# Kernel optimization log

Measured on AMD Instinct MI355X. Metric: run time of the kernel, lower is better.

## Reference

```python
import jax, jax.numpy as jnp
import numpy as np

N, K, A = 4096, 64, 8      # nodes, level-2 paths per node, attrs per l2-neighbor
D = 128                    # embed_dim
NU, NR, NA = 100000, 32, 5000  # user vocab, rating vocab, attribute vocab


def setup_inputs() -> dict:
    key = jax.random.key(0)
    ks = jax.random.split(key, 12)
    s = 0.02
    return dict(
        nodes=jax.random.randint(ks[0], (N,), 0, NU),
        paths_rel=jax.random.randint(ks[1], (N, K, 2), 0, NR),
        paths_nbr=jax.random.randint(ks[2], (N, K), 0, NU),
        attrs=jax.random.randint(ks[3], (N, K, A), 0, NA),
        u2e=jax.random.normal(ks[4], (NU, D), dtype=jnp.float32) * s,
        r2e=jax.random.normal(ks[5], (NR, D), dtype=jnp.float32) * s,
        ua2e=jax.random.normal(ks[6], (NA, D), dtype=jnp.float32) * s,
        W1=jax.random.normal(ks[7], (4 * D, 2 * D), dtype=jnp.float32) * s,
        b1=jnp.zeros((2 * D,), jnp.float32),
        W2=jax.random.normal(ks[8], (2 * D, D), dtype=jnp.float32) * s,
        b2=jnp.zeros((D,), jnp.float32),
        A1=jax.random.normal(ks[9], (2 * D, D), dtype=jnp.float32) * s,
        ab1=jnp.zeros((D,), jnp.float32),
        A2=jax.random.normal(ks[10], (D, D), dtype=jnp.float32) * s,
        ab2=jnp.zeros((D,), jnp.float32),
        A3=jax.random.normal(ks[11], (D, 1), dtype=jnp.float32) * s,
        ab3=jnp.zeros((1,), jnp.float32),
    )


def reference(nodes, paths_rel, paths_nbr, attrs, u2e, r2e, ua2e,
              W1, b1, W2, b2, A1, ab1, A2, ab2, A3, ab3):
    # per-path embedding gathers
    r1 = r2e[paths_rel[..., 0]]           # [N,K,D]
    r2 = r2e[paths_rel[..., 1]]           # [N,K,D]
    ne = u2e[paths_nbr]                   # [N,K,D]
    ae = ua2e[attrs].sum(axis=2)          # [N,K,A,D] -> [N,K,D] (uvAttrEmbedding sum)
    # concat + 2-layer MLP (w_r1, w_r2)
    x = jnp.concatenate([r1, r2, ne, ae], axis=-1)   # [N,K,4D]
    h = jax.nn.relu(x @ W1 + b1)                     # [N,K,2D]
    h = jax.nn.relu(h @ W2 + b2)                     # [N,K,D]
    # attention vs self embedding
    self_e = u2e[nodes]                              # [N,D]
    c = jnp.concatenate(
        [h, jnp.broadcast_to(self_e[:, None, :], h.shape)], axis=-1)  # [N,K,2D]
    a = jax.nn.relu(c @ A1 + ab1)
    a = jax.nn.relu(a @ A2 + ab2)
    logits = (a @ A3 + ab3)[..., 0]                  # [N,K]
    w = jax.nn.softmax(logits, axis=1)
    # attention-weighted reduce over paths
    return jnp.einsum('nk,nkd->nd', w, h)            # [N,D]
```

## Files before the change

### kernel.cpp

```cpp
#include <hip/hip_runtime.h>
#include <hip/hip_bf16.h>

#define NN 4096
#define KK 64
#define AA 8
#define DD 128

#define R1_SIZE   17408
#define XH_STRIDE 264
#define A_STRIDE  136
#define A2_OFF    8704
#define H2_STRIDE 136

typedef __bf16 bf16x8 __attribute__((ext_vector_type(8)));
typedef short  s16x8  __attribute__((ext_vector_type(8)));
typedef float  f32x4  __attribute__((ext_vector_type(4)));

__device__ __forceinline__ short f2bf(float f) {
    unsigned u = __builtin_bit_cast(unsigned, f);
    u += 0x7FFFu + ((u >> 16) & 1u);
    return (short)(u >> 16);
}
__device__ __forceinline__ float bf2f(short s) {
    unsigned u = ((unsigned)(unsigned short)s) << 16;
    return __builtin_bit_cast(float, u);
}
__device__ __forceinline__ void store_bf8(short* dst, float4 a, float4 b) {
    s16x8 v;
    v[0] = f2bf(a.x); v[1] = f2bf(a.y); v[2] = f2bf(a.z); v[3] = f2bf(a.w);
    v[4] = f2bf(b.x); v[5] = f2bf(b.y); v[6] = f2bf(b.z); v[7] = f2bf(b.w);
    *(s16x8*)dst = v;
}

__global__ void pack_all(const float* __restrict__ W1, const float* __restrict__ W2,
                         const float* __restrict__ A1, const float* __restrict__ A2,
                         short* __restrict__ W1p, short* __restrict__ W2p,
                         short* __restrict__ A1p, short* __restrict__ A2p)
{
    int t = blockIdx.x * 256 + threadIdx.x;
    const float* src; short* dst; int Ncols, ksl, idx;
    if (t < 131072)      { src = W1; dst = W1p; Ncols = 256; ksl = 4; idx = t; }
    else if (t < 163840) { src = W2; dst = W2p; Ncols = 128; ksl = 3; idx = t - 131072; }
    else if (t < 180224) { src = A1; dst = A1p; Ncols = 128; ksl = 2; idx = t - 163840; }
    else                 { src = A2; dst = A2p; Ncols = 128; ksl = 2; idx = t - 180224; }
    int j     = idx & 7;
    int lane  = (idx >> 3) & 63;
    int fi    = idx >> 9;
    int kstep = fi & ((1 << ksl) - 1);
    int ntile = fi >> ksl;
    int k  = kstep * 32 + (lane >> 4) * 8 + j;
    int nn = ntile * 16 + (lane & 15);
    dst[idx] = f2bf(src[(size_t)k * Ncols + nn]);
}

__global__ void prep_s1(const int* __restrict__ nodes, const float* __restrict__ u2e,
                        const float* __restrict__ A1, const float* __restrict__ ab1,
                        float* __restrict__ s1g)
{
    __shared__ float row[DD];
    const int n = blockIdx.x, c = threadIdx.x;
    const int node = nodes[n];
    row[c] = u2e[(size_t)node * DD + c];
    __syncthreads();
    float acc = ab1[c];
#pragma unroll 8
    for (int i = 0; i < DD; ++i)
        acc = fmaf(row[i], A1[(size_t)(DD + i) * DD + c], acc);
    s1g[(size_t)n * DD + c] = acc;
}

__launch_bounds__(256, 3)
__global__ void l2agg_mfma(
    const int* __restrict__ paths_rel,
    const int* __restrict__ paths_nbr,
    const int* __restrict__ attrs,
    const float* __restrict__ u2e,
    const float* __restrict__ r2e,
    const float* __restrict__ ua2e,
    const float* __restrict__ b1,
    const float* __restrict__ b2,
    const float* __restrict__ ab2,
    const float* __restrict__ A3,
    const float* __restrict__ ab3,
    const short* __restrict__ W1p,
    const short* __restrict__ W2p,
    const short* __restrict__ A1p,
    const short* __restrict__ A2p,
    const float* __restrict__ s1g,
    float* __restrict__ out)
{
    __shared__ short reg1[R1_SIZE];
    __shared__ short h2s[KK * H2_STRIDE];
    __shared__ int   idx_lds[KK * AA + KK];
    float* logits = (float*)&reg1[0];
    float* wts    = (float*)&reg1[128];

    const int n    = blockIdx.x;
    const int tid  = threadIdx.x;
    const int lane = tid & 63;
    const int wv   = tid >> 6;
    const int mr   = lane & 15;
    const int q    = lane >> 4;

    {
        const int* ab = attrs + (size_t)n * KK * AA;
        __builtin_amdgcn_global_load_lds(
            (const __attribute__((address_space(1))) void*)(ab + wv * 128 + lane),
            (__attribute__((address_space(3))) void*)(idx_lds + wv * 128), 4, 0, 0);
        __builtin_amdgcn_global_load_lds(
            (const __attribute__((address_space(1))) void*)(ab + wv * 128 + 64 + lane),
            (__attribute__((address_space(3))) void*)(idx_lds + wv * 128 + 64), 4, 0, 0);
        if (wv == 0) {
            const int* nb = paths_nbr + (size_t)n * KK;
            __builtin_amdgcn_global_load_lds(
                (const __attribute__((address_space(1))) void*)(nb + lane),
                (__attribute__((address_space(3))) void*)(idx_lds + 512), 4, 0, 0);
        }
    }

#pragma unroll
    for (int pass = 0; pass < 4; ++pass) {
        const int p  = pass * 16 + (tid >> 4);
        const int t  = tid & 15;
        const int o  = t * 8;
        const int pk = n * KK + p;
        const int i0 = paths_rel[pk * 2 + 0];
        const int i1 = paths_rel[pk * 2 + 1];
        float4 r1a = *(const float4*)&r2e[(size_t)i0 * DD + o];
        float4 r1b = *(const float4*)&r2e[(size_t)i0 * DD + o + 4];
        float4 r2a = *(const float4*)&r2e[(size_t)i1 * DD + o];
        float4 r2b = *(const float4*)&r2e[(size_t)i1 * DD + o + 4];
        store_bf8(&reg1[p * XH_STRIDE + o], r1a, r1b);
        store_bf8(&reg1[p * XH_STRIDE + 128 + o], r2a, r2b);
    }
    __syncthreads();

    const short* W1b = W1p + wv * 32768 + lane * 8;
    f32x4 acc1[4][4] = {};
    bf16x8 bfc[4], bfn[4];
#pragma unroll
    for (int nt = 0; nt < 4; ++nt) bfc[nt] = *(const bf16x8*)&W1b[nt * 8192];
#pragma unroll
    for (int ks = 0; ks < 8; ++ks) {
#pragma unroll
        for (int nt = 0; nt < 4; ++nt)
            bfn[nt] = *(const bf16x8*)&W1b[nt * 8192 + (ks + 1) * 512];
        bf16x8 af[4];
#pragma unroll
        for (int mt = 0; mt < 4; ++mt)
            af[mt] = *(const bf16x8*)&reg1[(mt * 16 + mr) * XH_STRIDE + ks * 32 + q * 8];
#pragma unroll
        for (int nt = 0; nt < 4; ++nt)
#pragma unroll
            for (int mt = 0; mt < 4; ++mt)
                acc1[mt][nt] = __builtin_amdgcn_mfma_f32_16x16x32_bf16(af[mt], bfc[nt], acc1[mt][nt], 0, 0, 0);
#pragma unroll
        for (int nt = 0; nt < 4; ++nt) bfc[nt] = bfn[nt];
    }
    __syncthreads();

#pragma unroll
    for (int pass = 0; pass < 4; ++pass) {
        const int p  = pass * 16 + (tid >> 4);
        const int t  = tid & 15;
        const int o  = t * 8;
        const int nb = idx_lds[512 + p];
        float4 nea = *(const float4*)&u2e[(size_t)nb * DD + o];
        float4 neb = *(const float4*)&u2e[(size_t)nb * DD + o + 4];
        float4 aea = make_float4(0.f, 0.f, 0.f, 0.f);
        float4 aeb = make_float4(0.f, 0.f, 0.f, 0.f);
#pragma unroll
        for (int a = 0; a < AA; ++a) {
            const int ai = idx_lds[p * AA + a];
            float4 va = *(const float4*)&ua2e[(size_t)ai * DD + o];
            float4 vb = *(const float4*)&ua2e[(size_t)ai * DD + o + 4];
            aea.x += va.x; aea.y += va.y; aea.z += va.z; aea.w += va.w;
            aeb.x += vb.x; aeb.y += vb.y; aeb.z += vb.z; aeb.w += vb.w;
        }
        store_bf8(&reg1[p * XH_STRIDE + o], nea, neb);
        store_bf8(&reg1[p * XH_STRIDE + 128 + o], aea, aeb);
    }
    __syncthreads();

#pragma unroll
    for (int ks = 8; ks < 16; ++ks) {
        if (ks < 15) {
#pragma unroll
            for (int nt = 0; nt < 4; ++nt)
                bfn[nt] = *(const bf16x8*)&W1b[nt * 8192 + (ks + 1) * 512];
        }
        bf16x8 af[4];
#pragma unroll
        for (int mt = 0; mt < 4; ++mt)
            af[mt] = *(const bf16x8*)&reg1[(mt * 16 + mr) * XH_STRIDE + (ks - 8) * 32 + q * 8];
#pragma unroll
        for (int nt = 0; nt < 4; ++nt)
#pragma unroll
            for (int mt = 0; mt < 4; ++mt)
                acc1[mt][nt] = __builtin_amdgcn_mfma_f32_16x16x32_bf16(af[mt], bfc[nt], acc1[mt][nt], 0, 0, 0);
        if (ks < 15) {
#pragma unroll
            for (int nt = 0; nt < 4; ++nt) bfc[nt] = bfn[nt];
        }
    }

    const short* W2b = W2p + wv * 8192 + lane * 8;
    bf16x8 g2c[2], g2n[2];
    g2c[0] = *(const bf16x8*)&W2b[0];
    g2c[1] = *(const bf16x8*)&W2b[4096];
    __syncthreads();

#pragma unroll
    for (int nt = 0; nt < 4; ++nt) {
        const int col = (wv * 4 + nt) * 16 + mr;
        const float bb = b1[col];
#pragma unroll
        for (int mt = 0; mt < 4; ++mt)
#pragma unroll
            for (int r = 0; r < 4; ++r)
                reg1[(mt * 16 + q * 4 + r) * XH_STRIDE + col] =
                    f2bf(fmaxf(acc1[mt][nt][r] + bb, 0.f));
    }
    __syncthreads();

    f32x4 acc2[4][2] = {};
#pragma unroll
    for (int ks = 0; ks < 8; ++ks) {
        if (ks < 7) {
            g2n[0] = *(const bf16x8*)&W2b[(ks + 1) * 512];
            g2n[1] = *(const bf16x8*)&W2b[4096 + (ks + 1) * 512];
        }
        bf16x8 af[4];
#pragma unroll
        for (int mt = 0; mt < 4; ++mt)
            af[mt] = *(const bf16x8*)&reg1[(mt * 16 + mr) * XH_STRIDE + ks * 32 + q * 8];
#pragma unroll
        for (int nt = 0; nt < 2; ++nt)
#pragma unroll
            for (int mt = 0; mt < 4; ++mt)
                acc2[mt][nt] = __builtin_amdgcn_mfma_f32_16x16x32_bf16(af[mt], g2c[nt], acc2[mt][nt], 0, 0, 0);
        if (ks < 7) { g2c[0] = g2n[0]; g2c[1] = g2n[1]; }
    }

    const short* A1b = A1p + wv * 4096 + lane * 8;
    bf16x8 g3f[2][4];
#pragma unroll
    for (int nt = 0; nt < 2; ++nt)
#pragma unroll
        for (int ks = 0; ks < 4; ++ks)
            g3f[nt][ks] = *(const bf16x8*)&A1b[nt * 2048 + ks * 512];
    float s1v[2];
    s1v[0] = s1g[(size_t)n * DD + (wv * 2 + 0) * 16 + mr];
    s1v[1] = s1g[(size_t)n * DD + (wv * 2 + 1) * 16 + mr];

#pragma unroll
    for (int nt = 0; nt < 2; ++nt) {
        const int col = (wv * 2 + nt) * 16 + mr;
        const float bb = b2[col];
#pragma unroll
        for (int mt = 0; mt < 4; ++mt)
#pragma unroll
            for (int r = 0; r < 4; ++r)
                h2s[(mt * 16 + q * 4 + r) * H2_STRIDE + col] =
                    f2bf(fmaxf(acc2[mt][nt][r] + bb, 0.f));
    }
    __syncthreads();

    {
        f32x4 acc[4][2];
#pragma unroll
        for (int nt = 0; nt < 2; ++nt)
#pragma unroll
            for (int mt = 0; mt < 4; ++mt) {
                acc[mt][nt][0] = s1v[nt]; acc[mt][nt][1] = s1v[nt];
                acc[mt][nt][2] = s1v[nt]; acc[mt][nt][3] = s1v[nt];
            }
#pragma unroll
        for (int ks = 0; ks < 4; ++ks) {
            bf16x8 af[4];
#pragma unroll
            for (int mt = 0; mt < 4; ++mt)
                af[mt] = *(const bf16x8*)&h2s[(mt * 16 + mr) * H2_STRIDE + ks * 32 + q * 8];
#pragma unroll
            for (int nt = 0; nt < 2; ++nt)
#pragma unroll
                for (int mt = 0; mt < 4; ++mt)
                    acc[mt][nt] = __builtin_amdgcn_mfma_f32_16x16x32_bf16(af[mt], g3f[nt][ks], acc[mt][nt], 0, 0, 0);
        }
        const short* A2b = A2p + wv * 4096 + lane * 8;
        bf16x8 g4f[2][4];
#pragma unroll
        for (int nt = 0; nt < 2; ++nt)
#pragma unroll
            for (int ks = 0; ks < 4; ++ks)
                g4f[nt][ks] = *(const bf16x8*)&A2b[nt * 2048 + ks * 512];

#pragma unroll
        for (int nt = 0; nt < 2; ++nt) {
            const int col = (wv * 2 + nt) * 16 + mr;
#pragma unroll
            for (int mt = 0; mt < 4; ++mt)
#pragma unroll
                for (int r = 0; r < 4; ++r)
                    reg1[(mt * 16 + q * 4 + r) * A_STRIDE + col] =
                        f2bf(fmaxf(acc[mt][nt][r], 0.f));
        }
        __syncthreads();

        f32x4 acc4[4][2];
#pragma unroll
        for (int nt = 0; nt < 2; ++nt) {
            const float bv = ab2[(wv * 2 + nt) * 16 + mr];
#pragma unroll
            for (int mt = 0; mt < 4; ++mt) {
                acc4[mt][nt][0] = bv; acc4[mt][nt][1] = bv;
                acc4[mt][nt][2] = bv; acc4[mt][nt][3] = bv;
            }
        }
#pragma unroll
        for (int ks = 0; ks < 4; ++ks) {
            bf16x8 af[4];
#pragma unroll
            for (int mt = 0; mt < 4; ++mt)
                af[mt] = *(const bf16x8*)&reg1[(mt * 16 + mr) * A_STRIDE + ks * 32 + q * 8];
#pragma unroll
            for (int nt = 0; nt < 2; ++nt)
#pragma unroll
                for (int mt = 0; mt < 4; ++mt)
                    acc4[mt][nt] = __builtin_amdgcn_mfma_f32_16x16x32_bf16(af[mt], g4f[nt][ks], acc4[mt][nt], 0, 0, 0);
        }
#pragma unroll
        for (int nt = 0; nt < 2; ++nt) {
            const int col = (wv * 2 + nt) * 16 + mr;
#pragma unroll
            for (int mt = 0; mt < 4; ++mt)
#pragma unroll
                for (int r = 0; r < 4; ++r)
                    reg1[A2_OFF + (mt * 16 + q * 4 + r) * A_STRIDE + col] =
                        f2bf(fmaxf(acc4[mt][nt][r], 0.f));
        }
    }
    __syncthreads();

    {
        const int t = tid & 15;
        float4 a3a = *(const float4*)&A3[t * 8];
        float4 a3b = *(const float4*)&A3[t * 8 + 4];
#pragma unroll
        for (int pass = 0; pass < 4; ++pass) {
            const int p = pass * 16 + (tid >> 4);
            const short* a2r = &reg1[A2_OFF + p * A_STRIDE];
            float part = bf2f(a2r[t * 8 + 0]) * a3a.x;
            part = fmaf(bf2f(a2r[t * 8 + 1]), a3a.y, part);
            part = fmaf(bf2f(a2r[t * 8 + 2]), a3a.z, part);
            part = fmaf(bf2f(a2r[t * 8 + 3]), a3a.w, part);
            part = fmaf(bf2f(a2r[t * 8 + 4]), a3b.x, part);
            part = fmaf(bf2f(a2r[t * 8 + 5]), a3b.y, part);
            part = fmaf(bf2f(a2r[t * 8 + 6]), a3b.z, part);
            part = fmaf(bf2f(a2r[t * 8 + 7]), a3b.w, part);
            part += __shfl_down(part, 8, 16);
            part += __shfl_down(part, 4, 16);
            part += __shfl_down(part, 2, 16);
            part += __shfl_down(part, 1, 16);
            if (t == 0) logits[p] = part + ab3[0];
        }
    }
    __syncthreads();

    if (tid < KK) {
        float l = logits[tid];
        float m = l;
#pragma unroll
        for (int off = 32; off > 0; off >>= 1) m = fmaxf(m, __shfl_xor(m, off, 64));
        float e = expf(l - m);
        float s = e;
#pragma unroll
        for (int off = 32; off > 0; off >>= 1) s += __shfl_xor(s, off, 64);
        wts[tid] = e / s;
    }
    __syncthreads();

    if (tid < DD) {
        float acc = 0.f;
#pragma unroll 8
        for (int k = 0; k < KK; ++k)
            acc = fmaf(wts[k], bf2f(h2s[k * H2_STRIDE + tid]), acc);
        out[(size_t)n * DD + tid] = acc;
    }
}

extern "C" void kernel_launch(void* const* d_in, const int* in_sizes, int n_in,
                              void* d_out, int out_size, void* d_ws, size_t ws_size,
                              hipStream_t stream)
{
    const int*   nodes     = (const int*)d_in[0];
    const int*   paths_rel = (const int*)d_in[1];
    const int*   paths_nbr = (const int*)d_in[2];
    const int*   attrs     = (const int*)d_in[3];
    const float* u2e  = (const float*)d_in[4];
    const float* r2e  = (const float*)d_in[5];
    const float* ua2e = (const float*)d_in[6];
    const float* W1   = (const float*)d_in[7];
    const float* b1   = (const float*)d_in[8];
    const float* W2   = (const float*)d_in[9];
    const float* b2   = (const float*)d_in[10];
    const float* A1   = (const float*)d_in[11];
    const float* ab1  = (const float*)d_in[12];
    const float* A2   = (const float*)d_in[13];
    const float* ab2  = (const float*)d_in[14];
    const float* A3   = (const float*)d_in[15];
    const float* ab3  = (const float*)d_in[16];
    float* out = (float*)d_out;

    short* wsp = (short*)d_ws;
    short* W1p = wsp;
    short* W2p = wsp + 131072;
    short* A1p = wsp + 163840;
    short* A2p = wsp + 180224;
    float* s1g = (float*)((char*)d_ws + 393216);

    hipLaunchKernelGGL(pack_all, dim3(768), dim3(256), 0, stream,
                       W1, W2, A1, A2, W1p, W2p, A1p, A2p);
    hipLaunchKernelGGL(prep_s1, dim3(NN), dim3(DD), 0, stream,
                       nodes, u2e, A1, ab1, s1g);
    hipLaunchKernelGGL(l2agg_mfma, dim3(NN), dim3(256), 0, stream,
                       paths_rel, paths_nbr, attrs, u2e, r2e, ua2e,
                       b1, b2, ab2, A3, ab3,
                       W1p, W2p, A1p, A2p, s1g, out);
}
```

Measured before the change: 334.3 us.

## Double block to 512 threads and fuse A3 logit reduction into registers

Moves the main kernel from 4 to 8 waves per block, so each wave computes half as many output column tiles in every MLP stage. This cuts per-thread accumulator and register use and spreads gather and MFMA work across more waves. The A3 dot product now runs straight from the A2 MFMA accumulators with cross-lane shuffles and per-wave partials, so the bf16 A2 activations are no longer written to and reread from LDS. In exchange each block needs more waves resident at once, and every wave reloads the same A-operand fragments from LDS, which raises LDS read traffic.

```diff
diff --git a/kernel.cpp b/kernel.cpp
--- a/kernel.cpp
+++ b/kernel.cpp
@@ -6,10 +6,9 @@
 #define AA 8
 #define DD 128
 
-#define R1_SIZE   17408
+#define R1_SIZE   16896
 #define XH_STRIDE 264
 #define A_STRIDE  136
-#define A2_OFF    8704
 #define H2_STRIDE 136
 
 typedef __bf16 bf16x8 __attribute__((ext_vector_type(8)));
@@ -69,7 +68,7 @@
     s1g[(size_t)n * DD + c] = acc;
 }
 
-__launch_bounds__(256, 3)
+__launch_bounds__(512, 4)
 __global__ void l2agg_mfma(
     const int* __restrict__ paths_rel,
     const int* __restrict__ paths_nbr,
@@ -92,8 +91,8 @@
     __shared__ short reg1[R1_SIZE];
     __shared__ short h2s[KK * H2_STRIDE];
     __shared__ int   idx_lds[KK * AA + KK];
-    float* logits = (float*)&reg1[0];
-    float* wts    = (float*)&reg1[128];
+    __shared__ float partials[8 * KK];
+    __shared__ float wts[KK];
 
     const int n    = blockIdx.x;
     const int tid  = threadIdx.x;
@@ -105,11 +104,8 @@
     {
         const int* ab = attrs + (size_t)n * KK * AA;
         __builtin_amdgcn_global_load_lds(
-            (const __attribute__((address_space(1))) void*)(ab + wv * 128 + lane),
-            (__attribute__((address_space(3))) void*)(idx_lds + wv * 128), 4, 0, 0);
-        __builtin_amdgcn_global_load_lds(
-            (const __attribute__((address_space(1))) void*)(ab + wv * 128 + 64 + lane),
-            (__attribute__((address_space(3))) void*)(idx_lds + wv * 128 + 64), 4, 0, 0);
+            (const __attribute__((address_space(1))) void*)(ab + wv * 64 + lane),
+            (__attribute__((address_space(3))) void*)(idx_lds + wv * 64), 4, 0, 0);
         if (wv == 0) {
             const int* nb = paths_nbr + (size_t)n * KK;
             __builtin_amdgcn_global_load_lds(
@@ -119,8 +115,8 @@
     }
 
 #pragma unroll
-    for (int pass = 0; pass < 4; ++pass) {
-        const int p  = pass * 16 + (tid >> 4);
+    for (int pass = 0; pass < 2; ++pass) {
+        const int p  = pass * 32 + (tid >> 4);
         const int t  = tid & 15;
         const int o  = t * 8;
         const int pk = n * KK + p;
@@ -135,33 +131,33 @@
     }
     __syncthreads();
 
-    const short* W1b = W1p + wv * 32768 + lane * 8;
-    f32x4 acc1[4][4] = {};
-    bf16x8 bfc[4], bfn[4];
-#pragma unroll
-    for (int nt = 0; nt < 4; ++nt) bfc[nt] = *(const bf16x8*)&W1b[nt * 8192];
+    const short* W1b = W1p + wv * 2 * 16 * 512 + lane * 8;
+    f32x4 acc1[4][2] = {};
+    bf16x8 bfc[2], bfn[2];
+#pragma unroll
+    for (int nt = 0; nt < 2; ++nt) bfc[nt] = *(const bf16x8*)&W1b[nt * 8192];
 #pragma unroll
     for (int ks = 0; ks < 8; ++ks) {
 #pragma unroll
-        for (int nt = 0; nt < 4; ++nt)
+        for (int nt = 0; nt < 2; ++nt)
             bfn[nt] = *(const bf16x8*)&W1b[nt * 8192 + (ks + 1) * 512];
         bf16x8 af[4];
 #pragma unroll
         for (int mt = 0; mt < 4; ++mt)
             af[mt] = *(const bf16x8*)&reg1[(mt * 16 + mr) * XH_STRIDE + ks * 32 + q * 8];
 #pragma unroll
-        for (int nt = 0; nt < 4; ++nt)
+        for (int nt = 0; nt < 2; ++nt)
 #pragma unroll
             for (int mt = 0; mt < 4; ++mt)
                 acc1[mt][nt] = __builtin_amdgcn_mfma_f32_16x16x32_bf16(af[mt], bfc[nt], acc1[mt][nt], 0, 0, 0);
 #pragma unroll
-        for (int nt = 0; nt < 4; ++nt) bfc[nt] = bfn[nt];
-    }
-    __syncthreads();
-
-#pragma unroll
-    for (int pass = 0; pass < 4; ++pass) {
-        const int p  = pass * 16 + (tid >> 4);
+        for (int nt = 0; nt < 2; ++nt) bfc[nt] = bfn[nt];
+    }
+    __syncthreads();
+
+#pragma unroll
+    for (int pass = 0; pass < 2; ++pass) {
+        const int p  = pass * 32 + (tid >> 4);
         const int t  = tid & 15;
         const int o  = t * 8;
         const int nb = idx_lds[512 + p];
@@ -186,7 +182,7 @@
     for (int ks = 8; ks < 16; ++ks) {
         if (ks < 15) {
 #pragma unroll
-            for (int nt = 0; nt < 4; ++nt)
+            for (int nt = 0; nt < 2; ++nt)
                 bfn[nt] = *(const bf16x8*)&W1b[nt * 8192 + (ks + 1) * 512];
         }
         bf16x8 af[4];
@@ -194,25 +190,23 @@
         for (int mt = 0; mt < 4; ++mt)
             af[mt] = *(const bf16x8*)&reg1[(mt * 16 + mr) * XH_STRIDE + (ks - 8) * 32 + q * 8];
 #pragma unroll
-        for (int nt = 0; nt < 4; ++nt)
+        for (int nt = 0; nt < 2; ++nt)
 #pragma unroll
             for (int mt = 0; mt < 4; ++mt)
                 acc1[mt][nt] = __builtin_amdgcn_mfma_f32_16x16x32_bf16(af[mt], bfc[nt], acc1[mt][nt], 0, 0, 0);
         if (ks < 15) {
 #pragma unroll
-            for (int nt = 0; nt < 4; ++nt) bfc[nt] = bfn[nt];
-        }
-    }
-
-    const short* W2b = W2p + wv * 8192 + lane * 8;
-    bf16x8 g2c[2], g2n[2];
-    g2c[0] = *(const bf16x8*)&W2b[0];
-    g2c[1] = *(const bf16x8*)&W2b[4096];
-    __syncthreads();
-
-#pragma unroll
-    for (int nt = 0; nt < 4; ++nt) {
-        const int col = (wv * 4 + nt) * 16 + mr;
+            for (int nt = 0; nt < 2; ++nt) bfc[nt] = bfn[nt];
+        }
+    }
+
+    const short* W2b = W2p + wv * 8 * 512 + lane * 8;
+    bf16x8 g2c = *(const bf16x8*)&W2b[0], g2n;
+    __syncthreads();
+
+#pragma unroll
+    for (int nt = 0; nt < 2; ++nt) {
+        const int col = (wv * 2 + nt) * 16 + mr;
         const float bb = b1[col];
 #pragma unroll
         for (int mt = 0; mt < 4; ++mt)
@@ -223,58 +217,44 @@
     }
     __syncthreads();
 
-    f32x4 acc2[4][2] = {};
+    f32x4 acc2[4] = {};
 #pragma unroll
     for (int ks = 0; ks < 8; ++ks) {
-        if (ks < 7) {
-            g2n[0] = *(const bf16x8*)&W2b[(ks + 1) * 512];
-            g2n[1] = *(const bf16x8*)&W2b[4096 + (ks + 1) * 512];
-        }
+        if (ks < 7) g2n = *(const bf16x8*)&W2b[(ks + 1) * 512];
         bf16x8 af[4];
 #pragma unroll
         for (int mt = 0; mt < 4; ++mt)
             af[mt] = *(const bf16x8*)&reg1[(mt * 16 + mr) * XH_STRIDE + ks * 32 + q * 8];
 #pragma unroll
-        for (int nt = 0; nt < 2; ++nt)
-#pragma unroll
-            for (int mt = 0; mt < 4; ++mt)
-                acc2[mt][nt] = __builtin_amdgcn_mfma_f32_16x16x32_bf16(af[mt], g2c[nt], acc2[mt][nt], 0, 0, 0);
-        if (ks < 7) { g2c[0] = g2n[0]; g2c[1] = g2n[1]; }
-    }
-
-    const short* A1b = A1p + wv * 4096 + lane * 8;
-    bf16x8 g3f[2][4];
-#pragma unroll
-    for (int nt = 0; nt < 2; ++nt)
-#pragma unroll
-        for (int ks = 0; ks < 4; ++ks)
-            g3f[nt][ks] = *(const bf16x8*)&A1b[nt * 2048 + ks * 512];
-    float s1v[2];
-    s1v[0] = s1g[(size_t)n * DD + (wv * 2 + 0) * 16 + mr];
-    s1v[1] = s1g[(size_t)n * DD + (wv * 2 + 1) * 16 + mr];
-
-#pragma unroll
-    for (int nt = 0; nt < 2; ++nt) {
-        const int col = (wv * 2 + nt) * 16 + mr;
+        for (int mt = 0; mt < 4; ++mt)
+            acc2[mt] = __builtin_amdgcn_mfma_f32_16x16x32_bf16(af[mt], g2c, acc2[mt], 0, 0, 0);
+        if (ks < 7) g2c = g2n;
+    }
+
+    const short* A1b = A1p + wv * 4 * 512 + lane * 8;
+    bf16x8 g3f[4];
+#pragma unroll
+    for (int ks = 0; ks < 4; ++ks) g3f[ks] = *(const bf16x8*)&A1b[ks * 512];
+    const float s1v = s1g[(size_t)n * DD + wv * 16 + mr];
+
+    {
+        const int col = wv * 16 + mr;
         const float bb = b2[col];
 #pragma unroll
         for (int mt = 0; mt < 4; ++mt)
 #pragma unroll
             for (int r = 0; r < 4; ++r)
                 h2s[(mt * 16 + q * 4 + r) * H2_STRIDE + col] =
-                    f2bf(fmaxf(acc2[mt][nt][r] + bb, 0.f));
+                    f2bf(fmaxf(acc2[mt][r] + bb, 0.f));
     }
     __syncthreads();
 
     {
-        f32x4 acc[4][2];
-#pragma unroll
-        for (int nt = 0; nt < 2; ++nt)
-#pragma unroll
-            for (int mt = 0; mt < 4; ++mt) {
-                acc[mt][nt][0] = s1v[nt]; acc[mt][nt][1] = s1v[nt];
-                acc[mt][nt][2] = s1v[nt]; acc[mt][nt][3] = s1v[nt];
-            }
+        f32x4 acc3[4];
+#pragma unroll
+        for (int mt = 0; mt < 4; ++mt) {
+            acc3[mt][0] = s1v; acc3[mt][1] = s1v; acc3[mt][2] = s1v; acc3[mt][3] = s1v;
+        }
 #pragma unroll
         for (int ks = 0; ks < 4; ++ks) {
             bf16x8 af[4];
@@ -282,39 +262,31 @@
             for (int mt = 0; mt < 4; ++mt)
                 af[mt] = *(const bf16x8*)&h2s[(mt * 16 + mr) * H2_STRIDE + ks * 32 + q * 8];
 #pragma unroll
-            for (int nt = 0; nt < 2; ++nt)
-#pragma unroll
-                for (int mt = 0; mt < 4; ++mt)
-                    acc[mt][nt] = __builtin_amdgcn_mfma_f32_16x16x32_bf16(af[mt], g3f[nt][ks], acc[mt][nt], 0, 0, 0);
-        }
-        const short* A2b = A2p + wv * 4096 + lane * 8;
-        bf16x8 g4f[2][4];
-#pragma unroll
-        for (int nt = 0; nt < 2; ++nt)
-#pragma unroll
-            for (int ks = 0; ks < 4; ++ks)
-                g4f[nt][ks] = *(const bf16x8*)&A2b[nt * 2048 + ks * 512];
-
-#pragma unroll
-        for (int nt = 0; nt < 2; ++nt) {
-            const int col = (wv * 2 + nt) * 16 + mr;
+            for (int mt = 0; mt < 4; ++mt)
+                acc3[mt] = __builtin_amdgcn_mfma_f32_16x16x32_bf16(af[mt], g3f[ks], acc3[mt], 0, 0, 0);
+        }
+        const short* A2b = A2p + wv * 4 * 512 + lane * 8;
+        bf16x8 g4f[4];
+#pragma unroll
+        for (int ks = 0; ks < 4; ++ks) g4f[ks] = *(const bf16x8*)&A2b[ks * 512];
+
+        {
+            const int col = wv * 16 + mr;
 #pragma unroll
             for (int mt = 0; mt < 4; ++mt)
 #pragma unroll
                 for (int r = 0; r < 4; ++r)
                     reg1[(mt * 16 + q * 4 + r) * A_STRIDE + col] =
-                        f2bf(fmaxf(acc[mt][nt][r], 0.f));
+                        f2bf(fmaxf(acc3[mt][r], 0.f));
         }
         __syncthreads();
 
-        f32x4 acc4[4][2];
-#pragma unroll
-        for (int nt = 0; nt < 2; ++nt) {
-            const float bv = ab2[(wv * 2 + nt) * 16 + mr];
+        f32x4 acc4[4];
+        {
+            const float bv = ab2[wv * 16 + mr];
 #pragma unroll
             for (int mt = 0; mt < 4; ++mt) {
-                acc4[mt][nt][0] = bv; acc4[mt][nt][1] = bv;
-                acc4[mt][nt][2] = bv; acc4[mt][nt][3] = bv;
+                acc4[mt][0] = bv; acc4[mt][1] = bv; acc4[mt][2] = bv; acc4[mt][3] = bv;
             }
         }
 #pragma unroll
@@ -324,51 +296,37 @@
             for (int mt = 0; mt < 4; ++mt)
                 af[mt] = *(const bf16x8*)&reg1[(mt * 16 + mr) * A_STRIDE + ks * 32 + q * 8];
 #pragma unroll
-            for (int nt = 0; nt < 2; ++nt)
-#pragma unroll
-                for (int mt = 0; mt < 4; ++mt)
-                    acc4[mt][nt] = __builtin_amdgcn_mfma_f32_16x16x32_bf16(af[mt], g4f[nt][ks], acc4[mt][nt], 0, 0, 0);
-        }
-#pragma unroll
-        for (int nt = 0; nt < 2; ++nt) {
-            const int col = (wv * 2 + nt) * 16 + mr;
+            for (int mt = 0; mt < 4; ++mt)
+                acc4[mt] = __builtin_amdgcn_mfma_f32_16x16x32_bf16(af[mt], g4f[ks], acc4[mt], 0, 0, 0);
+        }
+        const float av = A3[wv * 16 + mr];
+        float pl[4][4];
+#pragma unroll
+        for (int mt = 0; mt < 4; ++mt)
+#pragma unroll
+            for (int r = 0; r < 4; ++r)
+                pl[mt][r] = fmaxf(acc4[mt][r], 0.f) * av;
+#pragma unroll
+        for (int off = 1; off < 16; off <<= 1)
 #pragma unroll
             for (int mt = 0; mt < 4; ++mt)
 #pragma unroll
                 for (int r = 0; r < 4; ++r)
-                    reg1[A2_OFF + (mt * 16 + q * 4 + r) * A_STRIDE + col] =
-                        f2bf(fmaxf(acc4[mt][nt][r], 0.f));
-        }
-    }
-    __syncthreads();
-
-    {
-        const int t = tid & 15;
-        float4 a3a = *(const float4*)&A3[t * 8];
-        float4 a3b = *(const float4*)&A3[t * 8 + 4];
-#pragma unroll
-        for (int pass = 0; pass < 4; ++pass) {
-            const int p = pass * 16 + (tid >> 4);
-            const short* a2r = &reg1[A2_OFF + p * A_STRIDE];
-            float part = bf2f(a2r[t * 8 + 0]) * a3a.x;
-            part = fmaf(bf2f(a2r[t * 8 + 1]), a3a.y, part);
-            part = fmaf(bf2f(a2r[t * 8 + 2]), a3a.z, part);
-            part = fmaf(bf2f(a2r[t * 8 + 3]), a3a.w, part);
-            part = fmaf(bf2f(a2r[t * 8 + 4]), a3b.x, part);
-            part = fmaf(bf2f(a2r[t * 8 + 5]), a3b.y, part);
-            part = fmaf(bf2f(a2r[t * 8 + 6]), a3b.z, part);
-            part = fmaf(bf2f(a2r[t * 8 + 7]), a3b.w, part);
-            part += __shfl_down(part, 8, 16);
-            part += __shfl_down(part, 4, 16);
-            part += __shfl_down(part, 2, 16);
-            part += __shfl_down(part, 1, 16);
-            if (t == 0) logits[p] = part + ab3[0];
+                    pl[mt][r] += __shfl_xor(pl[mt][r], off, 64);
+        if (mr == 0) {
+#pragma unroll
+            for (int mt = 0; mt < 4; ++mt)
+#pragma unroll
+                for (int r = 0; r < 4; ++r)
+                    partials[wv * KK + mt * 16 + q * 4 + r] = pl[mt][r];
         }
     }
     __syncthreads();
 
     if (tid < KK) {
-        float l = logits[tid];
+        float l = ab3[0];
+#pragma unroll
+        for (int w = 0; w < 8; ++w) l += partials[w * KK + tid];
         float m = l;
 #pragma unroll
         for (int off = 32; off > 0; off >>= 1) m = fmaxf(m, __shfl_xor(m, off, 64));
@@ -423,7 +381,7 @@
                        W1, W2, A1, A2, W1p, W2p, A1p, A2p);
     hipLaunchKernelGGL(prep_s1, dim3(NN), dim3(DD), 0, stream,
                        nodes, u2e, A1, ab1, s1g);
-    hipLaunchKernelGGL(l2agg_mfma, dim3(NN), dim3(256), 0, stream,
+    hipLaunchKernelGGL(l2agg_mfma, dim3(NN), dim3(512), 0, stream,
                        paths_rel, paths_nbr, attrs, u2e, r2e, ua2e,
                        b1, b2, ab2, A3, ab3,
                        W1p, W2p, A1p, A2p, s1g, out);
```

Result: faster. 297.6 us (-11.0%).
